# Optimization experiments

Hardware: AMD Instinct MI355X
Metric: run time of the kernel (lower is better)

Reference implementation:

```python
import jax, jax.numpy as jnp
import numpy as np

B, S, D, H = 4, 2048, 1024, 16  # batch, seq, num_hiddens, heads
HD = D // H  # head dim = 64
MASK_VALUE = -1e6


def setup_inputs() -> dict:
    key = jax.random.key(0)
    ks = jax.random.split(key, 8)
    scale = 1.0 / np.sqrt(D)
    return {
        "queries": jax.random.normal(ks[0], (B, S, D), jnp.float32),
        "keys": jax.random.normal(ks[1], (B, S, D), jnp.float32),
        "values": jax.random.normal(ks[2], (B, S, D), jnp.float32),
        "valid_lens": jax.random.randint(ks[3], (B,), 1, S + 1, jnp.int32),
        # torch Linear weights: shape (out_features, in_features), y = x @ W.T
        "Wq": jax.random.uniform(ks[4], (D, D), jnp.float32, -scale, scale),
        "Wk": jax.random.uniform(ks[5], (D, D), jnp.float32, -scale, scale),
        "Wv": jax.random.uniform(ks[6], (D, D), jnp.float32, -scale, scale),
        "Wo": jax.random.uniform(ks[7], (D, D), jnp.float32, -scale, scale),
    }


def _split_heads(x):
    # (B, S, D) -> (B, H, S, HD)
    return x.reshape(B, S, H, HD).transpose(0, 2, 1, 3)


def reference(queries, keys, values, valid_lens, Wq, Wk, Wv, Wo):
    q = _split_heads(queries @ Wq.T)
    k = _split_heads(keys @ Wk.T)
    v = _split_heads(values @ Wv.T)
    scores = jnp.einsum("bhqd,bhkd->bhqk", q, k) / jnp.sqrt(jnp.float32(HD))
    # per-batch valid_len masks keys beyond valid_len (same for all heads/queries)
    key_pos = jnp.arange(S)
    mask = key_pos[None, None, None, :] < valid_lens[:, None, None, None]
    scores = jnp.where(mask, scores, MASK_VALUE)
    attn = jax.nn.softmax(scores, axis=-1)
    out = jnp.einsum("bhqk,bhkd->bhqd", attn, v)  # (B, H, S, HD)
    out = out.transpose(0, 2, 1, 3).reshape(B, S, D)
    return out @ Wo.T
```

## Files before the change

kernel.cpp:

```cpp
#include <hip/hip_runtime.h>

#define Bn 4
#define Sn 2048
#define Dn 1024
#define Hn 16
#define HDn 64

typedef unsigned short u16;
typedef unsigned int u32;
typedef __bf16 bf16x8 __attribute__((ext_vector_type(8)));
typedef float f32x4 __attribute__((ext_vector_type(4)));

__device__ __forceinline__ u32 pack_rne(float a, float b) {
    u32 ua = __float_as_uint(a); ua += 0x7fffu + ((ua >> 16) & 1u);
    u32 ub = __float_as_uint(b); ub += 0x7fffu + ((ub >> 16) & 1u);
    return __builtin_amdgcn_perm(ub, ua, 0x07060302u);
}
__device__ __forceinline__ u32 pack_trunc(float a, float b) {
    return __builtin_amdgcn_perm(__float_as_uint(b), __float_as_uint(a), 0x07060302u);
}

__device__ __forceinline__ void async_copy16(const u16* g, u16* l) {
    __builtin_amdgcn_global_load_lds(
        (__attribute__((address_space(1))) void*)(g),
        (__attribute__((address_space(3))) void*)(l), 16, 0, 0);
}

struct CvtArgs {
    const float* in[7];
    u16* out[7];
    int n4[7];
};
__global__ __launch_bounds__(256) void cvt_multi(CvtArgs a) {
    int s = blockIdx.y;
    const float4* in4 = (const float4*)a.in[s];
    uint2* out2 = (uint2*)a.out[s];
    int n4 = a.n4[s];
    int i = blockIdx.x * blockDim.x + threadIdx.x;
    int stride = gridDim.x * blockDim.x;
    for (; i < n4; i += stride) {
        float4 v = in4[i];
        out2[i] = make_uint2(pack_rne(v.x, v.y), pack_rne(v.z, v.w));
    }
}

struct GemmArgs {
    const u16* A[3];
    const u16* Bw[3];
    void* C[3];
    float scale[3];
    int mode[3];
};
__global__ __launch_bounds__(256) void gemm_bf16(GemmArgs g) {
    __shared__ alignas(16) u16 As[128 * 32];
    __shared__ alignas(16) u16 Bs[128 * 32];
    int z = blockIdx.z;
    const u16* A = g.A[z];
    const u16* Bw = g.Bw[z];
    void* Cout = g.C[z];
    float scale = g.scale[z];
    int mode = g.mode[z];

    int t = threadIdx.x;
    int w = t >> 6, lane = t & 63;
    int lane15 = lane & 15, quad = lane >> 4;
    int wr = w >> 1, wc = w & 1;
    int row0 = blockIdx.y * 128, col0 = blockIdx.x * 128;

    const u16* PA = (mode == 1) ? Bs : As;
    const u16* PB = (mode == 1) ? As : Bs;
    int abase = (mode == 1) ? wc * 64 : wr * 64;
    int bbase = (mode == 1) ? wr * 64 : wc * 64;

    f32x4 acc[4][4];
#pragma unroll
    for (int mt = 0; mt < 4; ++mt)
#pragma unroll
        for (int nt = 0; nt < 4; ++nt)
            acc[mt][nt] = f32x4{0.f, 0.f, 0.f, 0.f};

    for (int k0 = 0; k0 < 1024; k0 += 32) {
        __syncthreads();
#pragma unroll
        for (int i = 0; i < 2; ++i) {
            int e = i * 2048 + t * 8;
            int r = e >> 5, c = e & 31;
            const u16* ga = A + (size_t)(row0 + r) * 1024 + k0 + c;
            const u16* gb = Bw + (size_t)(col0 + r) * 1024 + k0 + c;
            async_copy16(ga, &As[i * 2048 + w * 512]);
            async_copy16(gb, &Bs[i * 2048 + w * 512]);
        }
        __syncthreads();

        bf16x8 af[4], bf[4];
#pragma unroll
        for (int mt = 0; mt < 4; ++mt)
            af[mt] = *(const bf16x8*)&PA[(abase + mt * 16 + lane15) * 32 + quad * 8];
#pragma unroll
        for (int nt = 0; nt < 4; ++nt)
            bf[nt] = *(const bf16x8*)&PB[(bbase + nt * 16 + lane15) * 32 + quad * 8];
#pragma unroll
        for (int mt = 0; mt < 4; ++mt)
#pragma unroll
            for (int nt = 0; nt < 4; ++nt)
                acc[mt][nt] = __builtin_amdgcn_mfma_f32_16x16x32_bf16(
                    af[mt], bf[nt], acc[mt][nt], 0, 0, 0);
    }

#pragma unroll
    for (int mt = 0; mt < 4; ++mt)
#pragma unroll
        for (int nt = 0; nt < 4; ++nt) {
            if (mode == 1) {
                int f0 = col0 + wc * 64 + mt * 16 + quad * 4;
                int tok = row0 + wr * 64 + nt * 16 + lane15;
                int bb = tok >> 11, ss = tok & 2047;
                int hh = f0 >> 6, dd = f0 & 63;
                u32 w0 = pack_rne(acc[mt][nt][0] * scale, acc[mt][nt][1] * scale);
                u32 w1 = pack_rne(acc[mt][nt][2] * scale, acc[mt][nt][3] * scale);
                u16* p = (u16*)Cout + (((size_t)bb * Hn + hh) * Sn + ss) * HDn + dd;
                *(uint2*)p = make_uint2(w0, w1);
            } else if (mode == 3) {
                int n = col0 + wc * 64 + nt * 16 + lane15;
                int m0 = row0 + wr * 64 + mt * 16 + quad * 4;
                int bb = m0 >> 11, ss = m0 & 2047;
                int hh = n >> 6, dd = n & 63;
                u32 w0 = pack_rne(acc[mt][nt][0] * scale, acc[mt][nt][1] * scale);
                u32 w1 = pack_rne(acc[mt][nt][2] * scale, acc[mt][nt][3] * scale);
                u16* p = (u16*)Cout + (((size_t)bb * Hn + hh) * HDn + dd) * Sn + ss;
                *(uint2*)p = make_uint2(w0, w1);
            } else {
                int n = col0 + wc * 64 + nt * 16 + lane15;
                int m0 = row0 + wr * 64 + mt * 16 + quad * 4;
#pragma unroll
                for (int reg = 0; reg < 4; ++reg)
                    ((float*)Cout)[(size_t)(m0 + reg) * 1024 + n] =
                        acc[mt][nt][reg] * scale;
            }
        }
}

__global__ __launch_bounds__(256, 4) void attn_kernel(const u16* __restrict__ Qh,
                                                      const u16* __restrict__ Kh,
                                                      const u16* __restrict__ Vtg,
                                                      const int* __restrict__ valid_lens,
                                                      u16* __restrict__ O) {
    __shared__ alignas(16) u16 Ks[64 * 72];
    __shared__ alignas(16) u16 Vt[64 * 72];

    int t = threadIdx.x;
    int w = t >> 6, lane = t & 63;
    int lane15 = lane & 15, quad = lane >> 4;

    u32 raw = blockIdx.x;
    int qt = raw >> 6;
    int h = (raw >> 2) & 15;
    int b = (raw & 3) ^ ((raw >> 8) & 3);
    int bh = b * Hn + h;
    int q0 = qt * 128;
    int vl = valid_lens[b];
    int ntiles = (vl + 63) >> 6;

    const u16* Qb = Qh + (size_t)bh * (Sn * HDn);
    const u16* Kb = Kh + (size_t)bh * (Sn * HDn);
    const u16* Vb = Vtg + (size_t)bh * (HDn * Sn);

    int sr = t >> 3;
    int sc8 = (t & 7) * 8;
    int va = t & 7;
    int vcb = ((va & 4) << 3) | ((va & 1) << 4) | ((va & 2) << 1);

    bf16x8 qf[2][2];
#pragma unroll
    for (int nt = 0; nt < 2; ++nt)
#pragma unroll
        for (int kc = 0; kc < 2; ++kc)
            qf[nt][kc] = *(const bf16x8*)(Qb + (size_t)(q0 + w * 32 + nt * 16 + lane15) * HDn +
                                          kc * 32 + quad * 8);

    f32x4 oacc[4][2], lacc[2];
#pragma unroll
    for (int mt = 0; mt < 4; ++mt)
#pragma unroll
        for (int nt = 0; nt < 2; ++nt)
            oacc[mt][nt] = f32x4{0.f, 0.f, 0.f, 0.f};
    lacc[0] = f32x4{0.f, 0.f, 0.f, 0.f};
    lacc[1] = f32x4{0.f, 0.f, 0.f, 0.f};

    union { u32 u[4]; bf16x8 v; } ones;
    ones.u[0] = ones.u[1] = ones.u[2] = ones.u[3] = 0x3F803F80u;

    uint4 kpre[2], vpre[2];
#pragma unroll
    for (int p = 0; p < 2; ++p) {
        kpre[p] = *(const uint4*)(Kb + (size_t)(p * 32 + sr) * HDn + sc8);
        vpre[p] = *(const uint4*)(Vb + (size_t)(p * 32 + sr) * Sn + sc8);
    }

    for (int kt = 0; kt < ntiles; ++kt) {
        int kbase = kt * 64;
        __syncthreads();
#pragma unroll
        for (int p = 0; p < 2; ++p) {
            *(uint4*)&Ks[(p * 32 + sr) * 72 + sc8] = kpre[p];
            int drow = (p * 32 + sr) * 72;
            *(uint2*)&Vt[drow + vcb] = make_uint2(vpre[p].x, vpre[p].y);
            *(uint2*)&Vt[drow + vcb + 8] = make_uint2(vpre[p].z, vpre[p].w);
        }
        __syncthreads();

        int nkb = (kt + 1 < ntiles) ? kbase + 64 : kbase;
#pragma unroll
        for (int p = 0; p < 2; ++p) {
            kpre[p] = *(const uint4*)(Kb + (size_t)(nkb + p * 32 + sr) * HDn + sc8);
            vpre[p] = *(const uint4*)(Vb + (size_t)(p * 32 + sr) * Sn + nkb + sc8);
        }

        f32x4 sc[4][2];
#pragma unroll
        for (int mt = 0; mt < 4; ++mt) {
            bf16x8 kf0 = *(const bf16x8*)&Ks[(mt * 16 + lane15) * 72 + quad * 8];
            bf16x8 kf1 = *(const bf16x8*)&Ks[(mt * 16 + lane15) * 72 + 32 + quad * 8];
#pragma unroll
            for (int nt = 0; nt < 2; ++nt) {
                f32x4 s = f32x4{0.f, 0.f, 0.f, 0.f};
                s = __builtin_amdgcn_mfma_f32_16x16x32_bf16(kf0, qf[nt][0], s, 0, 0, 0);
                s = __builtin_amdgcn_mfma_f32_16x16x32_bf16(kf1, qf[nt][1], s, 0, 0, 0);
                sc[mt][nt] = s;
            }
        }

        if (kbase + 64 > vl) {
#pragma unroll
            for (int mt = 0; mt < 4; ++mt)
#pragma unroll
                for (int reg = 0; reg < 4; ++reg) {
                    int key = kbase + mt * 16 + quad * 4 + reg;
                    if (key >= vl) {
                        sc[mt][0][reg] = -1e30f;
                        sc[mt][1][reg] = -1e30f;
                    }
                }
        }

#pragma unroll
        for (int mt = 0; mt < 4; ++mt)
#pragma unroll
            for (int nt = 0; nt < 2; ++nt)
#pragma unroll
                for (int reg = 0; reg < 4; ++reg)
                    sc[mt][nt][reg] = __builtin_amdgcn_exp2f(sc[mt][nt][reg]);

        union { u32 u[4]; bf16x8 v; } pv[2][2];
#pragma unroll
        for (int nt = 0; nt < 2; ++nt) {
            pv[nt][0].u[0] = pack_trunc(sc[0][nt][0], sc[0][nt][1]);
            pv[nt][0].u[1] = pack_trunc(sc[0][nt][2], sc[0][nt][3]);
            pv[nt][0].u[2] = pack_trunc(sc[1][nt][0], sc[1][nt][1]);
            pv[nt][0].u[3] = pack_trunc(sc[1][nt][2], sc[1][nt][3]);
            pv[nt][1].u[0] = pack_trunc(sc[2][nt][0], sc[2][nt][1]);
            pv[nt][1].u[1] = pack_trunc(sc[2][nt][2], sc[2][nt][3]);
            pv[nt][1].u[2] = pack_trunc(sc[3][nt][0], sc[3][nt][1]);
            pv[nt][1].u[3] = pack_trunc(sc[3][nt][2], sc[3][nt][3]);
            lacc[nt] = __builtin_amdgcn_mfma_f32_16x16x32_bf16(
                ones.v, pv[nt][0].v, lacc[nt], 0, 0, 0);
            lacc[nt] = __builtin_amdgcn_mfma_f32_16x16x32_bf16(
                ones.v, pv[nt][1].v, lacc[nt], 0, 0, 0);
        }

#pragma unroll
        for (int mt = 0; mt < 4; ++mt) {
            bf16x8 vf0 = *(const bf16x8*)&Vt[(mt * 16 + lane15) * 72 + quad * 8];
            bf16x8 vf1 = *(const bf16x8*)&Vt[(mt * 16 + lane15) * 72 + 32 + quad * 8];
#pragma unroll
            for (int nt = 0; nt < 2; ++nt) {
                oacc[mt][nt] = __builtin_amdgcn_mfma_f32_16x16x32_bf16(
                    vf0, pv[nt][0].v, oacc[mt][nt], 0, 0, 0);
                oacc[mt][nt] = __builtin_amdgcn_mfma_f32_16x16x32_bf16(
                    vf1, pv[nt][1].v, oacc[mt][nt], 0, 0, 0);
            }
        }
    }

    float rl[2];
    rl[0] = __builtin_amdgcn_rcpf(lacc[0][0]);
    rl[1] = __builtin_amdgcn_rcpf(lacc[1][0]);
#pragma unroll
    for (int mt = 0; mt < 4; ++mt)
#pragma unroll
        for (int nt = 0; nt < 2; ++nt) {
            int q = q0 + w * 32 + nt * 16 + lane15;
            int d = h * HDn + mt * 16 + quad * 4;
            u32 w0 = pack_rne(oacc[mt][nt][0] * rl[nt], oacc[mt][nt][1] * rl[nt]);
            u32 w1 = pack_rne(oacc[mt][nt][2] * rl[nt], oacc[mt][nt][3] * rl[nt]);
            *(uint2*)&O[((size_t)b * Sn + q) * Dn + d] = make_uint2(w0, w1);
        }
}

extern "C" void kernel_launch(void* const* d_in, const int* in_sizes, int n_in,
                              void* d_out, int out_size, void* d_ws, size_t ws_size,
                              hipStream_t stream) {
    const float* q  = (const float*)d_in[0];
    const float* k  = (const float*)d_in[1];
    const float* v  = (const float*)d_in[2];
    const int*   vl = (const int*)d_in[3];
    const float* Wq = (const float*)d_in[4];
    const float* Wk = (const float*)d_in[5];
    const float* Wv = (const float*)d_in[6];
    const float* Wo = (const float*)d_in[7];

    u16* ws = (u16*)d_ws;
    const size_t NE = (size_t)Bn * Sn * Dn;
    const size_t NW = (size_t)Dn * Dn;
    const float qscale = 0.125f * 1.44269504f;
    const int M = Bn * Sn;
    dim3 gg(Dn / 128, M / 128);

    if (ws_size >= (6 * NE + 4 * NW) * 2) {
        u16* Qh  = ws;
        u16* Kh  = Qh + NE;
        u16* Vh  = Kh + NE;
        u16* Xq  = Vh + NE;
        u16* Xk  = Xq + NE;
        u16* Xv  = Xk + NE;
        u16* Wqb = Xv + NE;
        u16* Wkb = Wqb + NW;
        u16* Wvb = Wkb + NW;
        u16* Wob = Wvb + NW;
        u16* Ob  = Xq;

        CvtArgs ca;
        ca.in[0] = q;  ca.out[0] = Xq;  ca.n4[0] = (int)(NE / 4);
        ca.in[1] = k;  ca.out[1] = Xk;  ca.n4[1] = (int)(NE / 4);
        ca.in[2] = v;  ca.out[2] = Xv;  ca.n4[2] = (int)(NE / 4);
        ca.in[3] = Wq; ca.out[3] = Wqb; ca.n4[3] = (int)(NW / 4);
        ca.in[4] = Wk; ca.out[4] = Wkb; ca.n4[4] = (int)(NW / 4);
        ca.in[5] = Wv; ca.out[5] = Wvb; ca.n4[5] = (int)(NW / 4);
        ca.in[6] = Wo; ca.out[6] = Wob; ca.n4[6] = (int)(NW / 4);
        cvt_multi<<<dim3(512, 7), 256, 0, stream>>>(ca);

        GemmArgs gp;
        gp.A[0] = Xq; gp.Bw[0] = Wqb; gp.C[0] = Qh; gp.scale[0] = qscale; gp.mode[0] = 1;
        gp.A[1] = Xk; gp.Bw[1] = Wkb; gp.C[1] = Kh; gp.scale[1] = 1.0f;   gp.mode[1] = 1;
        gp.A[2] = Xv; gp.Bw[2] = Wvb; gp.C[2] = Vh; gp.scale[2] = 1.0f;   gp.mode[2] = 3;
        gemm_bf16<<<dim3(gg.x, gg.y, 3), 256, 0, stream>>>(gp);

        attn_kernel<<<dim3(1024), 256, 0, stream>>>(Qh, Kh, Vh, vl, Ob);

        GemmArgs go;
        for (int i = 0; i < 3; ++i) {
            go.A[i] = Ob; go.Bw[i] = Wob; go.C[i] = d_out;
            go.scale[i] = 1.0f; go.mode[i] = 2;
        }
        gemm_bf16<<<dim3(gg.x, gg.y, 1), 256, 0, stream>>>(go);
    } else {
        u16* Qh  = ws;
        u16* Kh  = Qh + NE;
        u16* Vh  = Kh + NE;
        u16* Xb  = Vh + NE;
        u16* Wqb = Xb + NE;
        u16* Wkb = Wqb + NW;
        u16* Wvb = Wkb + NW;
        u16* Wob = Wvb + NW;
        u16* Ob  = Wob + NW;

        CvtArgs cw;
        cw.in[0] = Wq; cw.out[0] = Wqb; cw.n4[0] = (int)(NW / 4);
        cw.in[1] = Wk; cw.out[1] = Wkb; cw.n4[1] = (int)(NW / 4);
        cw.in[2] = Wv; cw.out[2] = Wvb; cw.n4[2] = (int)(NW / 4);
        cw.in[3] = Wo; cw.out[3] = Wob; cw.n4[3] = (int)(NW / 4);
        for (int i = 4; i < 7; ++i) { cw.in[i] = Wq; cw.out[i] = Wqb; cw.n4[i] = 0; }
        cvt_multi<<<dim3(512, 4), 256, 0, stream>>>(cw);

        const float* xs[3] = {q, k, v};
        u16* outs[3] = {Qh, Kh, Vh};
        const u16* wbs[3] = {Wqb, Wkb, Wvb};
        float scs[3] = {qscale, 1.0f, 1.0f};
        int mds[3] = {1, 1, 3};
        for (int i = 0; i < 3; ++i) {
            CvtArgs cx;
            cx.in[0] = xs[i]; cx.out[0] = Xb; cx.n4[0] = (int)(NE / 4);
            for (int j = 1; j < 7; ++j) { cx.in[j] = xs[i]; cx.out[j] = Xb; cx.n4[j] = 0; }
            cvt_multi<<<dim3(512, 1), 256, 0, stream>>>(cx);
            GemmArgs gp;
            for (int j = 0; j < 3; ++j) {
                gp.A[j] = Xb; gp.Bw[j] = wbs[i]; gp.C[j] = outs[i];
                gp.scale[j] = scs[i]; gp.mode[j] = mds[i];
            }
            gemm_bf16<<<dim3(gg.x, gg.y, 1), 256, 0, stream>>>(gp);
        }

        attn_kernel<<<dim3(1024), 256, 0, stream>>>(Qh, Kh, Vh, vl, Ob);

        GemmArgs go;
        for (int j = 0; j < 3; ++j) {
            go.A[j] = Ob; go.Bw[j] = Wob; go.C[j] = d_out;
            go.scale[j] = 1.0f; go.mode[j] = 2;
        }
        gemm_bf16<<<dim3(gg.x, gg.y, 1), 256, 0, stream>>>(go);
    }
}
```

Measured before the change: 330.0 us.

## Double GEMM K-tile to 64 with XOR-swizzled LDS and vectorized fp32 output

The bf16 GEMM now stages 64-wide K slices per iteration instead of 32, which halves the number of barrier pairs. It applies an XOR swizzle to the LDS layout to avoid bank conflicts on the fragment reads. The grid is flattened so the Q/K/V projections interleave by blockIdx, and the output projection uses the swapped operand order so each lane can write float4 instead of scalar strided stores. LDS use per block doubles, which could affect occupancy.

```diff
diff --git a/kernel.cpp b/kernel.cpp
--- a/kernel.cpp
+++ b/kernel.cpp
@@ -51,10 +51,15 @@
     float scale[3];
     int mode[3];
 };
-__global__ __launch_bounds__(256) void gemm_bf16(GemmArgs g) {
-    __shared__ alignas(16) u16 As[128 * 32];
-    __shared__ alignas(16) u16 Bs[128 * 32];
-    int z = blockIdx.z;
+__global__ __launch_bounds__(256) void gemm_bf16(GemmArgs g, int nz) {
+    __shared__ alignas(16) u16 As[128 * 64];
+    __shared__ alignas(16) u16 Bs[128 * 64];
+    u32 id = blockIdx.x;
+    int z = id % nz;
+    u32 r2 = id / nz;
+    int row0 = (int)(r2 >> 3) * 128;
+    int col0 = (int)(r2 & 7) * 128;
+
     const u16* A = g.A[z];
     const u16* Bw = g.Bw[z];
     void* Cout = g.C[z];
@@ -65,12 +70,13 @@
     int w = t >> 6, lane = t & 63;
     int lane15 = lane & 15, quad = lane >> 4;
     int wr = w >> 1, wc = w & 1;
-    int row0 = blockIdx.y * 128, col0 = blockIdx.x * 128;
-
-    const u16* PA = (mode == 1) ? Bs : As;
-    const u16* PB = (mode == 1) ? As : Bs;
-    int abase = (mode == 1) ? wc * 64 : wr * 64;
-    int bbase = (mode == 1) ? wr * 64 : wc * 64;
+    int sr = t >> 3, sg = t & 7;
+
+    bool swapped = (mode != 3);
+    const u16* PA = swapped ? Bs : As;
+    const u16* PB = swapped ? As : Bs;
+    int abase = swapped ? wc * 64 : wr * 64;
+    int bbase = swapped ? wr * 64 : wc * 64;
 
     f32x4 acc[4][4];
 #pragma unroll
@@ -79,32 +85,39 @@
         for (int nt = 0; nt < 4; ++nt)
             acc[mt][nt] = f32x4{0.f, 0.f, 0.f, 0.f};
 
-    for (int k0 = 0; k0 < 1024; k0 += 32) {
+    for (int k0 = 0; k0 < 1024; k0 += 64) {
         __syncthreads();
 #pragma unroll
-        for (int i = 0; i < 2; ++i) {
-            int e = i * 2048 + t * 8;
-            int r = e >> 5, c = e & 31;
-            const u16* ga = A + (size_t)(row0 + r) * 1024 + k0 + c;
-            const u16* gb = Bw + (size_t)(col0 + r) * 1024 + k0 + c;
+        for (int i = 0; i < 4; ++i) {
+            int r = i * 32 + sr;
+            int gc = ((sg ^ (r & 7)) << 3);
+            const u16* ga = A + (size_t)(row0 + r) * 1024 + k0 + gc;
+            const u16* gb = Bw + (size_t)(col0 + r) * 1024 + k0 + gc;
             async_copy16(ga, &As[i * 2048 + w * 512]);
             async_copy16(gb, &Bs[i * 2048 + w * 512]);
         }
         __syncthreads();
 
-        bf16x8 af[4], bf[4];
-#pragma unroll
-        for (int mt = 0; mt < 4; ++mt)
-            af[mt] = *(const bf16x8*)&PA[(abase + mt * 16 + lane15) * 32 + quad * 8];
-#pragma unroll
-        for (int nt = 0; nt < 4; ++nt)
-            bf[nt] = *(const bf16x8*)&PB[(bbase + nt * 16 + lane15) * 32 + quad * 8];
-#pragma unroll
-        for (int mt = 0; mt < 4; ++mt)
-#pragma unroll
-            for (int nt = 0; nt < 4; ++nt)
-                acc[mt][nt] = __builtin_amdgcn_mfma_f32_16x16x32_bf16(
-                    af[mt], bf[nt], acc[mt][nt], 0, 0, 0);
+#pragma unroll
+        for (int kc = 0; kc < 2; ++kc) {
+            bf16x8 af[4], bf[4];
+#pragma unroll
+            for (int mt = 0; mt < 4; ++mt) {
+                int r = abase + mt * 16 + lane15;
+                af[mt] = *(const bf16x8*)&PA[r * 64 + (((kc * 4 + quad) ^ (r & 7)) << 3)];
+            }
+#pragma unroll
+            for (int nt = 0; nt < 4; ++nt) {
+                int r = bbase + nt * 16 + lane15;
+                bf[nt] = *(const bf16x8*)&PB[r * 64 + (((kc * 4 + quad) ^ (r & 7)) << 3)];
+            }
+#pragma unroll
+            for (int mt = 0; mt < 4; ++mt)
+#pragma unroll
+                for (int nt = 0; nt < 4; ++nt)
+                    acc[mt][nt] = __builtin_amdgcn_mfma_f32_16x16x32_bf16(
+                        af[mt], bf[nt], acc[mt][nt], 0, 0, 0);
+        }
     }
 
 #pragma unroll
@@ -120,7 +133,13 @@
                 u32 w1 = pack_rne(acc[mt][nt][2] * scale, acc[mt][nt][3] * scale);
                 u16* p = (u16*)Cout + (((size_t)bb * Hn + hh) * Sn + ss) * HDn + dd;
                 *(uint2*)p = make_uint2(w0, w1);
-            } else if (mode == 3) {
+            } else if (mode == 2) {
+                int f0 = col0 + wc * 64 + mt * 16 + quad * 4;
+                int tok = row0 + wr * 64 + nt * 16 + lane15;
+                float4 o = make_float4(acc[mt][nt][0] * scale, acc[mt][nt][1] * scale,
+                                       acc[mt][nt][2] * scale, acc[mt][nt][3] * scale);
+                *(float4*)((float*)Cout + (size_t)tok * 1024 + f0) = o;
+            } else {
                 int n = col0 + wc * 64 + nt * 16 + lane15;
                 int m0 = row0 + wr * 64 + mt * 16 + quad * 4;
                 int bb = m0 >> 11, ss = m0 & 2047;
@@ -129,13 +148,6 @@
                 u32 w1 = pack_rne(acc[mt][nt][2] * scale, acc[mt][nt][3] * scale);
                 u16* p = (u16*)Cout + (((size_t)bb * Hn + hh) * HDn + dd) * Sn + ss;
                 *(uint2*)p = make_uint2(w0, w1);
-            } else {
-                int n = col0 + wc * 64 + nt * 16 + lane15;
-                int m0 = row0 + wr * 64 + mt * 16 + quad * 4;
-#pragma unroll
-                for (int reg = 0; reg < 4; ++reg)
-                    ((float*)Cout)[(size_t)(m0 + reg) * 1024 + n] =
-                        acc[mt][nt][reg] * scale;
             }
         }
 }
@@ -313,8 +325,6 @@
     const size_t NE = (size_t)Bn * Sn * Dn;
     const size_t NW = (size_t)Dn * Dn;
     const float qscale = 0.125f * 1.44269504f;
-    const int M = Bn * Sn;
-    dim3 gg(Dn / 128, M / 128);
 
     if (ws_size >= (6 * NE + 4 * NW) * 2) {
         u16* Qh  = ws;
@@ -343,7 +353,7 @@
         gp.A[0] = Xq; gp.Bw[0] = Wqb; gp.C[0] = Qh; gp.scale[0] = qscale; gp.mode[0] = 1;
         gp.A[1] = Xk; gp.Bw[1] = Wkb; gp.C[1] = Kh; gp.scale[1] = 1.0f;   gp.mode[1] = 1;
         gp.A[2] = Xv; gp.Bw[2] = Wvb; gp.C[2] = Vh; gp.scale[2] = 1.0f;   gp.mode[2] = 3;
-        gemm_bf16<<<dim3(gg.x, gg.y, 3), 256, 0, stream>>>(gp);
+        gemm_bf16<<<dim3(512 * 3), 256, 0, stream>>>(gp, 3);
 
         attn_kernel<<<dim3(1024), 256, 0, stream>>>(Qh, Kh, Vh, vl, Ob);
 
@@ -352,7 +362,7 @@
             go.A[i] = Ob; go.Bw[i] = Wob; go.C[i] = d_out;
             go.scale[i] = 1.0f; go.mode[i] = 2;
         }
-        gemm_bf16<<<dim3(gg.x, gg.y, 1), 256, 0, stream>>>(go);
+        gemm_bf16<<<dim3(512), 256, 0, stream>>>(go, 1);
     } else {
         u16* Qh  = ws;
         u16* Kh  = Qh + NE;
@@ -387,7 +397,7 @@
                 gp.A[j] = Xb; gp.Bw[j] = wbs[i]; gp.C[j] = outs[i];
                 gp.scale[j] = scs[i]; gp.mode[j] = mds[i];
             }
-            gemm_bf16<<<dim3(gg.x, gg.y, 1), 256, 0, stream>>>(gp);
+            gemm_bf16<<<dim3(512), 256, 0, stream>>>(gp, 1);
         }
 
         attn_kernel<<<dim3(1024), 256, 0, stream>>>(Qh, Kh, Vh, vl, Ob);
@@ -397,6 +407,6 @@
             go.A[j] = Ob; go.Bw[j] = Wob; go.C[j] = d_out;
             go.scale[j] = 1.0f; go.mode[j] = 2;
         }
-        gemm_bf16<<<dim3(gg.x, gg.y, 1), 256, 0, stream>>>(go);
+        gemm_bf16<<<dim3(512), 256, 0, stream>>>(go, 1);
     }
 }
```

New measurement: 333.4 us. Within noise of the previous version (+1.0%).
